# Performance work log

Hardware: AMD Instinct MI355X
Metric: run time of the kernel (lower is better)

## Reference

```python
import jax, jax.numpy as jnp
import numpy as np

B, T = 16, 8192
L, RC, DC, SC, EC, E, NC = 16, 32, 32, 256, 256, 100, 256


def conv1d(x, w, b, dilation=1):
    # x: [B, Cin, T], w: [Cout, Cin, K], b: [Cout]
    y = jax.lax.conv_general_dilated(
        x, w, window_strides=(1,), padding='VALID',
        rhs_dilation=(dilation,), dimension_numbers=('NCH', 'OIH', 'NCH'))
    return y + b[None, :, None]


def setup_inputs() -> dict:
    key = jax.random.key(0)
    ks = jax.random.split(key, 32)
    n = lambda k, shp: (jax.random.normal(k, shp) * 0.1).astype(jnp.float32)
    return dict(
        tokens=jax.random.randint(ks[0], (B, T), 0, NC),
        emb=n(ks[1], (NC, E)),
        init_w=n(ks[2], (RC, E, 1)), init_b=n(ks[3], (RC,)),
        dil_w=n(ks[4], (L, DC, RC, 2)), dil_b=n(ks[5], (L, DC)),
        filt_w=n(ks[6], (L, DC, DC, 2)), filt_b=n(ks[7], (L, DC)),
        gate_w=n(ks[8], (L, DC, DC, 2)), gate_b=n(ks[9], (L, DC)),
        res_w=n(ks[10], (L, RC, DC, 1)), res_b=n(ks[11], (L, RC)),
        skip_w=n(ks[12], (L, SC, DC, 1)), skip_b=n(ks[13], (L, SC)),
        end1_w=n(ks[14], (EC, SC, 1)), end1_b=n(ks[15], (EC,)),
        end2_w=n(ks[16], (EC, EC, 1)), end2_b=n(ks[17], (EC,)),
        fc1_w=n(ks[18], (128, 256)), fc1_b=n(ks[19], (128,)),
        fc2_w=n(ks[20], (128, 128)), fc2_b=n(ks[21], (128,)),
        fc3_w=n(ks[22], (64, 128)), fc3_b=n(ks[23], (64,)),
        fc4_w=n(ks[24], (NC, 64)), fc4_b=n(ks[25], (NC,)),
    )


def reference(tokens, emb, init_w, init_b, dil_w, dil_b, filt_w, filt_b,
              gate_w, gate_b, res_w, res_b, skip_w, skip_b,
              end1_w, end1_b, end2_w, end2_b,
              fc1_w, fc1_b, fc2_w, fc2_b, fc3_w, fc3_b, fc4_w, fc4_b):
    x = emb[tokens]                     # [B, T, E]
    x = jnp.transpose(x, (0, 2, 1))     # [B, E, T]
    x = conv1d(x, init_w, init_b)       # [B, RC, T]
    skip = None
    for i in range(L):
        d = 2 ** (i % 4)                # dilation resets each block of 4 layers
        xp = jnp.pad(x, ((0, 0), (0, 0), (d + 1, 0)))        # left pad d+1
        residual = conv1d(xp, dil_w[i], dil_b[i], dilation=d)  # [B, DC, T+1]
        f = jnp.tanh(conv1d(residual, filt_w[i], filt_b[i]))   # [B, DC, T]
        g = jax.nn.sigmoid(conv1d(residual, gate_w[i], gate_b[i]))
        x = f * g
        skip = conv1d(x, skip_w[i], skip_b[i])   # overwritten each layer (source bug, kept faithful)
        x = conv1d(x, res_w[i], res_b[i]) + residual[:, :, :-1]
    h = jax.nn.relu(conv1d(jax.nn.relu(skip), end1_w, end1_b))
    h = conv1d(h, end2_w, end2_b)       # [B, EC, T]
    h = h[:, :, -1]                     # [B, 256] last timestep only
    h = jax.nn.relu(h @ fc1_w.T + fc1_b)
    h = jax.nn.relu(h @ fc2_w.T + fc2_b)
    h = jax.nn.relu(h @ fc3_w.T + fc3_b)
    out = h @ fc4_w.T + fc4_b           # [B, NC]
    return out
```

## Files before the change

kernel.cpp:

```cpp
#include <hip/hip_runtime.h>


#define BB 16
#define TT 8192
#define LL 16
#define W0 77
#define NT 256

typedef __attribute__((ext_vector_type(8)))  short short8;
typedef __attribute__((ext_vector_type(16))) float float16;

#define MFMA_B16(a, b, c) __builtin_amdgcn_mfma_f32_32x32x16_bf16(a, b, c, 0, 0, 0)

__device__ __forceinline__ short f2bs(float f) {
  union { float ff; unsigned u; } v; v.ff = f;
  unsigned u = v.u;
  return (short)((u + 0x7FFFu + ((u >> 16) & 1u)) >> 16);
}
__device__ __forceinline__ float b2f(short h) {
  union { unsigned u; float f; } v;
  v.u = ((unsigned)(unsigned short)h) << 16; return v.f;
}
__device__ __forceinline__ float fast_sigmoid(float x) {
  return 1.f / (1.f + __expf(-x));
}
__device__ __forceinline__ float fast_tanh(float x) {
  return 2.f / (1.f + __expf(-2.f * x)) - 1.f;
}

__device__ __forceinline__ void afrag2(const short* src, int row, int kh, short8* out) {
  out[0] = *(const short8*)&src[row * 32 + 8 * kh];
  out[1] = *(const short8*)&src[row * 32 + 16 + 8 * kh];
}

__device__ __forceinline__ void stage_weights(
    int li, short* dst,
    const float* dil_w, const float* filt_w, const float* gate_w, const float* res_w,
    int t0, int nthr)
{
  for (int cid = t0; cid < 896; cid += nthr) {
    int mat = cid >> 7;
    int rem = cid & 127;
    int h = rem >> 6, ln = rem & 63;
    int n = ln & 31, k2 = ln >> 5;
    int base = (li * 32 + n) * 32 + 16 * h + 8 * k2;
    short8 v;
    if (mat == 6) {
      const float* p = res_w + base;
      #pragma unroll
      for (int j = 0; j < 8; j++) v[j] = f2bs(p[j]);
    } else {
      const float* w = (mat < 2) ? dil_w : (mat < 4) ? filt_w : gate_w;
      const float* p = w + base * 2 + (mat & 1);
      #pragma unroll
      for (int j = 0; j < 8; j++) v[j] = f2bs(p[2 * j]);
    }
    *(short8*)&dst[((mat * 2 + h) * 64 + ln) * 8] = v;
  }
}

__global__ __launch_bounds__(NT, 1) void wavenet_kernel(
    const int* __restrict__ tokens,
    const float* __restrict__ emb,
    const float* __restrict__ init_w, const float* __restrict__ init_b,
    const float* __restrict__ dil_w,  const float* __restrict__ dil_b,
    const float* __restrict__ filt_w, const float* __restrict__ filt_b,
    const float* __restrict__ gate_w, const float* __restrict__ gate_b,
    const float* __restrict__ res_w,  const float* __restrict__ res_b,
    const float* __restrict__ skip_w, const float* __restrict__ skip_b,
    const float* __restrict__ end1_w, const float* __restrict__ end1_b,
    const float* __restrict__ end2_w, const float* __restrict__ end2_b,
    const float* __restrict__ fc1_w,  const float* __restrict__ fc1_b,
    const float* __restrict__ fc2_w,  const float* __restrict__ fc2_b,
    const float* __restrict__ fc3_w,  const float* __restrict__ fc3_b,
    const float* __restrict__ fc4_w,  const float* __restrict__ fc4_b,
    float* __restrict__ out)
{
  __shared__ __align__(16) short bfw[2][7168];
  __shared__ float bias2[2][128];
  __shared__ __align__(16) short xbuf[W0 * 32];
  __shared__ __align__(16) short pool[8624];
  __shared__ int tok[W0];
  __shared__ float vecA[256], vecB[256];

  short* rb = pool;
  short* xm = pool + 2432;

  const int tid  = threadIdx.x;
  const int lane = tid & 63;
  const int wv   = tid >> 6;
  const int m    = lane & 31;
  const int kh   = lane >> 5;
  const int b    = blockIdx.x;

  if (tid < W0) tok[tid] = tokens[b * TT + (TT - 1 - tid)];
  __syncthreads();

  for (int cid = tid; cid < 77 * 14; cid += NT) {
    int u = cid / 14, s = cid % 14;
    const float* er = emb + tok[u] * 100 + s * 8;
    short8 v;
    if (s < 12) {
      #pragma unroll
      for (int j = 0; j < 8; j++) v[j] = f2bs(er[j]);
    } else if (s == 12) {
      #pragma unroll
      for (int j = 0; j < 4; j++) v[j] = f2bs(er[j]);
      #pragma unroll
      for (int j = 4; j < 8; j++) v[j] = 0;
    } else {
      #pragma unroll
      for (int j = 0; j < 8; j++) v[j] = 0;
    }
    *(short8*)&pool[u * 112 + s * 8] = v;
  }
  stage_weights(0, bfw[0], dil_w, filt_w, gate_w, res_w, tid, NT);
  if (tid < 128) {
    const float* bsrc = (tid < 32) ? dil_b : (tid < 64) ? filt_b : (tid < 96) ? gate_b : res_b;
    bias2[0][tid] = bsrc[tid & 31];
  }
  __syncthreads();

  if (wv == 0) {
    short8 bi[7];
    #pragma unroll
    for (int s = 0; s < 7; s++) {
      const float* p = init_w + m * 100 + s * 16 + kh * 8;
      short8 v;
      if (s < 6) {
        #pragma unroll
        for (int j = 0; j < 8; j++) v[j] = f2bs(p[j]);
      } else if (kh == 0) {
        #pragma unroll
        for (int j = 0; j < 4; j++) v[j] = f2bs(p[j]);
        #pragma unroll
        for (int j = 4; j < 8; j++) v[j] = 0;
      } else {
        #pragma unroll
        for (int j = 0; j < 8; j++) v[j] = 0;
      }
      bi[s] = v;
    }
    const float binit = init_b[m];
    int u = 0;
    #pragma unroll
    for (int t = 0; t < 3; t++) {
      int R = t * 32;
      u = R + m; if (u > 76) u = 76;
      float16 acc;
      #pragma unroll
      for (int r = 0; r < 16; r++) acc[r] = binit;
      #pragma unroll
      for (int s = 0; s < 7; s++) {
        short8 a = *(const short8*)&pool[u * 112 + s * 16 + kh * 8];
        acc = MFMA_B16(a, bi[s], acc);
      }
      #pragma unroll
      for (int r = 0; r < 16; r++) {
        int row = (r & 3) + 8 * (r >> 2) + 4 * kh;
        int uu = R + row;
        if (uu < W0) xbuf[uu * 32 + m] = f2bs(acc[r]);
      }
    }
  }

  int Win = W0;
  for (int i = 0; i < LL; i++) {
    __syncthreads();
    const int d = 1 << (i & 3);
    const int Wout = Win - d - 1;
    if (wv == 0) {
      const short* bw = bfw[i & 1];
      const float* bs = bias2[i & 1];
      short8 BW[7][2];
      #pragma unroll
      for (int mat = 0; mat < 7; mat++)
        #pragma unroll
        for (int h = 0; h < 2; h++)
          BW[mat][h] = *(const short8*)&bw[((mat * 2 + h) * 64 + lane) * 8];
      const int T1 = (Wout + 32) >> 5;
      const int T2 = (Wout + 31) >> 5;

      for (int t = 0; t < T1; t++) {
        int R = t * 32;
        int vra = R + m + d; if (vra > Win - 1) vra = Win - 1;
        int vrz = R + m;     if (vrz > Win - 1) vrz = Win - 1;
        short8 aA[2], aZ[2];
        afrag2(xbuf, vra, kh, aA);
        afrag2(xbuf, vrz, kh, aZ);
        float16 acc;
        const float bc = bs[m];
        #pragma unroll
        for (int r = 0; r < 16; r++) acc[r] = bc;
        acc = MFMA_B16(aA[0], BW[0][0], acc);
        acc = MFMA_B16(aA[1], BW[0][1], acc);
        acc = MFMA_B16(aZ[0], BW[1][0], acc);
        acc = MFMA_B16(aZ[1], BW[1][1], acc);
        #pragma unroll
        for (int r = 0; r < 16; r++) {
          int row = (r & 3) + 8 * (r >> 2) + 4 * kh;
          int vr = R + row;
          if (vr <= Wout) rb[vr * 32 + m] = f2bs(acc[r]);
        }
      }
      asm volatile("s_waitcnt lgkmcnt(0)" ::: "memory");

      for (int t = 0; t < T2; t++) {
        int R = t * 32;
        int r1 = R + m + 1; if (r1 > Wout) r1 = Wout;
        int r0 = R + m;     if (r0 > Wout) r0 = Wout;
        short8 a1[2], a0[2];
        afrag2(rb, r1, kh, a1);
        afrag2(rb, r0, kh, a0);
        float16 accF, accG;
        const float bf = bs[32 + m], bg = bs[64 + m];
        #pragma unroll
        for (int r = 0; r < 16; r++) { accF[r] = bf; accG[r] = bg; }
        accF = MFMA_B16(a1[0], BW[2][0], accF);
        accF = MFMA_B16(a1[1], BW[2][1], accF);
        accF = MFMA_B16(a0[0], BW[3][0], accF);
        accF = MFMA_B16(a0[1], BW[3][1], accF);
        accG = MFMA_B16(a1[0], BW[4][0], accG);
        accG = MFMA_B16(a1[1], BW[4][1], accG);
        accG = MFMA_B16(a0[0], BW[5][0], accG);
        accG = MFMA_B16(a0[1], BW[5][1], accG);
        #pragma unroll
        for (int r = 0; r < 16; r++) {
          int row = (r & 3) + 8 * (r >> 2) + 4 * kh;
          int uf = R + row;
          if (uf < Wout)
            xm[uf * 32 + m] = f2bs(fast_tanh(accF[r]) * fast_sigmoid(accG[r]));
        }
      }
      asm volatile("s_waitcnt lgkmcnt(0)" ::: "memory");

      for (int t = 0; t < T2; t++) {
        int R = t * 32;
        int rx = R + m; if (rx > Wout - 1) rx = Wout - 1;
        short8 aX[2];
        afrag2(xm, rx, kh, aX);
        float16 accX;
        const float br = bs[96 + m];
        #pragma unroll
        for (int r = 0; r < 16; r++) {
          int row = (r & 3) + 8 * (r >> 2) + 4 * kh;
          int rr = R + row + 1; if (rr > Wout) rr = Wout;
          accX[r] = br + b2f(rb[rr * 32 + m]);
        }
        accX = MFMA_B16(aX[0], BW[6][0], accX);
        accX = MFMA_B16(aX[1], BW[6][1], accX);
        #pragma unroll
        for (int r = 0; r < 16; r++) {
          int row = (r & 3) + 8 * (r >> 2) + 4 * kh;
          int uf = R + row;
          if (uf < Wout) xbuf[uf * 32 + m] = f2bs(accX[r]);
        }
      }
      asm volatile("s_waitcnt lgkmcnt(0)" ::: "memory");
    } else if (i + 1 < LL) {
      stage_weights(i + 1, bfw[(i + 1) & 1], dil_w, filt_w, gate_w, res_w,
                    tid - 64, 192);
      int idx = tid - 64;
      if (idx < 128) {
        const float* bsrc = (idx < 32) ? dil_b : (idx < 64) ? filt_b : (idx < 96) ? gate_b : res_b;
        bias2[(i + 1) & 1][idx] = bsrc[(i + 1) * 32 + (idx & 31)];
      }
    }
    Win = Wout;
  }
  __syncthreads();

  {
    float acc = skip_b[15 * 256 + tid];
    const float* wr = skip_w + (15 * 256 + tid) * 32;
    #pragma unroll
    for (int k = 0; k < 32; k += 4) {
      float4 w = *(const float4*)&wr[k];
      acc += (w.x * b2f(xm[k]) + w.y * b2f(xm[k+1])) + (w.z * b2f(xm[k+2]) + w.w * b2f(xm[k+3]));
    }
    vecA[tid] = fmaxf(acc, 0.f);
  }
  __syncthreads();
  {
    const float* wr = end1_w + tid * 256;
    float a4[4] = {0.f, 0.f, 0.f, 0.f};
    #pragma unroll 4
    for (int k = 0; k < 256; k += 16) {
      #pragma unroll
      for (int q = 0; q < 4; q++) {
        float4 w = *(const float4*)&wr[k + 4 * q];
        a4[q] += (w.x * vecA[k+4*q] + w.y * vecA[k+4*q+1]) + (w.z * vecA[k+4*q+2] + w.w * vecA[k+4*q+3]);
      }
    }
    vecB[tid] = fmaxf(end1_b[tid] + (a4[0] + a4[1]) + (a4[2] + a4[3]), 0.f);
  }
  __syncthreads();
  float h2;
  {
    const float* wr = end2_w + tid * 256;
    float a4[4] = {0.f, 0.f, 0.f, 0.f};
    #pragma unroll 4
    for (int k = 0; k < 256; k += 16) {
      #pragma unroll
      for (int q = 0; q < 4; q++) {
        float4 w = *(const float4*)&wr[k + 4 * q];
        a4[q] += (w.x * vecB[k+4*q] + w.y * vecB[k+4*q+1]) + (w.z * vecB[k+4*q+2] + w.w * vecB[k+4*q+3]);
      }
    }
    h2 = end2_b[tid] + (a4[0] + a4[1]) + (a4[2] + a4[3]);
  }
  __syncthreads();
  vecA[tid] = h2;
  __syncthreads();
  if (tid < 128) {
    const float* wr = fc1_w + tid * 256;
    float a4[4] = {0.f, 0.f, 0.f, 0.f};
    #pragma unroll 4
    for (int k = 0; k < 256; k += 16) {
      #pragma unroll
      for (int q = 0; q < 4; q++) {
        float4 w = *(const float4*)&wr[k + 4 * q];
        a4[q] += (w.x * vecA[k+4*q] + w.y * vecA[k+4*q+1]) + (w.z * vecA[k+4*q+2] + w.w * vecA[k+4*q+3]);
      }
    }
    vecB[tid] = fmaxf(fc1_b[tid] + (a4[0] + a4[1]) + (a4[2] + a4[3]), 0.f);
  }
  __syncthreads();
  if (tid < 128) {
    const float* wr = fc2_w + tid * 128;
    float a4[4] = {0.f, 0.f, 0.f, 0.f};
    #pragma unroll 2
    for (int k = 0; k < 128; k += 16) {
      #pragma unroll
      for (int q = 0; q < 4; q++) {
        float4 w = *(const float4*)&wr[k + 4 * q];
        a4[q] += (w.x * vecB[k+4*q] + w.y * vecB[k+4*q+1]) + (w.z * vecB[k+4*q+2] + w.w * vecB[k+4*q+3]);
      }
    }
    vecA[tid] = fmaxf(fc2_b[tid] + (a4[0] + a4[1]) + (a4[2] + a4[3]), 0.f);
  }
  __syncthreads();
  if (tid < 64) {
    const float* wr = fc3_w + tid * 128;
    float a4[4] = {0.f, 0.f, 0.f, 0.f};
    #pragma unroll 2
    for (int k = 0; k < 128; k += 16) {
      #pragma unroll
      for (int q = 0; q < 4; q++) {
        float4 w = *(const float4*)&wr[k + 4 * q];
        a4[q] += (w.x * vecA[k+4*q] + w.y * vecA[k+4*q+1]) + (w.z * vecA[k+4*q+2] + w.w * vecA[k+4*q+3]);
      }
    }
    vecB[tid] = fmaxf(fc3_b[tid] + (a4[0] + a4[1]) + (a4[2] + a4[3]), 0.f);
  }
  __syncthreads();
  {
    const float* wr = fc4_w + tid * 64;
    float a4[4] = {0.f, 0.f, 0.f, 0.f};
    #pragma unroll
    for (int k = 0; k < 64; k += 16) {
      #pragma unroll
      for (int q = 0; q < 4; q++) {
        float4 w = *(const float4*)&wr[k + 4 * q];
        a4[q] += (w.x * vecB[k+4*q] + w.y * vecB[k+4*q+1]) + (w.z * vecB[k+4*q+2] + w.w * vecB[k+4*q+3]);
      }
    }
    out[b * 256 + tid] = fc4_b[tid] + (a4[0] + a4[1]) + (a4[2] + a4[3]);
  }
}

extern "C" void kernel_launch(void* const* d_in, const int* in_sizes, int n_in,
                              void* d_out, int out_size, void* d_ws, size_t ws_size,
                              hipStream_t stream) {
  wavenet_kernel<<<BB, NT, 0, stream>>>(
      (const int*)d_in[0],    (const float*)d_in[1],  (const float*)d_in[2],  (const float*)d_in[3],
      (const float*)d_in[4],  (const float*)d_in[5],  (const float*)d_in[6],  (const float*)d_in[7],
      (const float*)d_in[8],  (const float*)d_in[9],  (const float*)d_in[10], (const float*)d_in[11],
      (const float*)d_in[12], (const float*)d_in[13], (const float*)d_in[14], (const float*)d_in[15],
      (const float*)d_in[16], (const float*)d_in[17], (const float*)d_in[18], (const float*)d_in[19],
      (const float*)d_in[20], (const float*)d_in[21], (const float*)d_in[22], (const float*)d_in[23],
      (const float*)d_in[24], (const float*)d_in[25], (float*)d_out);
}
```

Measured before the change: 228.9 us.

## Split layer time tiles across waves and prefetch next-layer weights into registers

Each layer's 32-row time tiles are now processed in parallel, one wave per tile, instead of wave 0 looping over them while the other waves only staged weights. Next-layer weights and biases are loaded from global memory into registers by all threads before the compute. They are converted to bf16 and written to shared memory afterwards, so the load latency overlaps with the MFMA work. This targets the serialized single-wave critical path in this latency-bound kernel, at the cost of an extra block barrier per layer and higher register pressure.

Result: faster. 212.2 us (-7.3%).

```diff
diff --git a/kernel.cpp b/kernel.cpp
--- a/kernel.cpp
+++ b/kernel.cpp
@@ -33,29 +33,23 @@
   out[1] = *(const short8*)&src[row * 32 + 16 + 8 * kh];
 }
 
-__device__ __forceinline__ void stage_weights(
-    int li, short* dst,
-    const float* dil_w, const float* filt_w, const float* gate_w, const float* res_w,
-    int t0, int nthr)
+__device__ __forceinline__ void load_chunk(
+    int li, int cid, float* pf,
+    const float* dil_w, const float* filt_w, const float* gate_w, const float* res_w)
 {
-  for (int cid = t0; cid < 896; cid += nthr) {
-    int mat = cid >> 7;
-    int rem = cid & 127;
-    int h = rem >> 6, ln = rem & 63;
-    int n = ln & 31, k2 = ln >> 5;
-    int base = (li * 32 + n) * 32 + 16 * h + 8 * k2;
-    short8 v;
-    if (mat == 6) {
-      const float* p = res_w + base;
-      #pragma unroll
-      for (int j = 0; j < 8; j++) v[j] = f2bs(p[j]);
-    } else {
-      const float* w = (mat < 2) ? dil_w : (mat < 4) ? filt_w : gate_w;
-      const float* p = w + base * 2 + (mat & 1);
-      #pragma unroll
-      for (int j = 0; j < 8; j++) v[j] = f2bs(p[2 * j]);
-    }
-    *(short8*)&dst[((mat * 2 + h) * 64 + ln) * 8] = v;
+  int mat = cid >> 7;
+  int h = (cid >> 6) & 1, ln = cid & 63;
+  int n = ln & 31, k2 = ln >> 5;
+  int base = (li * 32 + n) * 32 + 16 * h + 8 * k2;
+  if (mat == 6) {
+    const float* p = res_w + base;
+    #pragma unroll
+    for (int j = 0; j < 8; j++) pf[j] = p[j];
+  } else {
+    const float* w = (mat < 2) ? dil_w : (mat < 4) ? filt_w : gate_w;
+    const float* p = w + base * 2 + (mat & 1);
+    #pragma unroll
+    for (int j = 0; j < 8; j++) pf[j] = p[2 * j];
   }
 }
 
@@ -114,7 +108,14 @@
     }
     *(short8*)&pool[u * 112 + s * 8] = v;
   }
-  stage_weights(0, bfw[0], dil_w, filt_w, gate_w, res_w, tid, NT);
+  for (int cid = tid; cid < 896; cid += NT) {
+    float pf[8];
+    load_chunk(0, cid, pf, dil_w, filt_w, gate_w, res_w);
+    short8 v;
+    #pragma unroll
+    for (int j = 0; j < 8; j++) v[j] = f2bs(pf[j]);
+    *(short8*)&bfw[0][cid * 8] = v;
+  }
   if (tid < 128) {
     const float* bsrc = (tid < 32) ? dil_b : (tid < 64) ? filt_b : (tid < 96) ? gate_b : res_b;
     bias2[0][tid] = bsrc[tid & 31];
@@ -142,11 +143,10 @@
       bi[s] = v;
     }
     const float binit = init_b[m];
-    int u = 0;
     #pragma unroll
     for (int t = 0; t < 3; t++) {
       int R = t * 32;
-      u = R + m; if (u > 76) u = 76;
+      int u = R + m; if (u > 76) u = 76;
       float16 acc;
       #pragma unroll
       for (int r = 0; r < 16; r++) acc[r] = binit;
@@ -163,112 +163,132 @@
       }
     }
   }
+  __syncthreads();
 
   int Win = W0;
   for (int i = 0; i < LL; i++) {
-    __syncthreads();
     const int d = 1 << (i & 3);
     const int Wout = Win - d - 1;
-    if (wv == 0) {
-      const short* bw = bfw[i & 1];
-      const float* bs = bias2[i & 1];
-      short8 BW[7][2];
-      #pragma unroll
-      for (int mat = 0; mat < 7; mat++)
+    const int T = (Wout + 32) >> 5;
+    const short* bw = bfw[i & 1];
+    const float* bs = bias2[i & 1];
+
+    float pf[4][8];
+    float pbias = 0.f;
+    const int nch = (tid < 128) ? 4 : 3;
+    if (i + 1 < LL) {
+      #pragma unroll
+      for (int q = 0; q < 4; q++) {
+        if (q < nch)
+          load_chunk(i + 1, tid + q * NT, pf[q], dil_w, filt_w, gate_w, res_w);
+      }
+      if (tid < 128) {
+        const float* bsrc = (tid < 32) ? dil_b : (tid < 64) ? filt_b : (tid < 96) ? gate_b : res_b;
+        pbias = bsrc[(i + 1) * 32 + (tid & 31)];
+      }
+    }
+
+    if (wv < T) {
+      const int R = wv * 32;
+      short8 B0[2], B1[2];
+      #pragma unroll
+      for (int h = 0; h < 2; h++) {
+        B0[h] = *(const short8*)&bfw[i & 1][((0 * 2 + h) * 64 + lane) * 8];
+        B1[h] = *(const short8*)&bfw[i & 1][((1 * 2 + h) * 64 + lane) * 8];
+      }
+      int vra = R + m + d; if (vra > Win - 1) vra = Win - 1;
+      int vrz = R + m;     if (vrz > Win - 1) vrz = Win - 1;
+      short8 aA[2], aZ[2];
+      afrag2(xbuf, vra, kh, aA);
+      afrag2(xbuf, vrz, kh, aZ);
+      float16 acc;
+      const float bc = bs[m];
+      #pragma unroll
+      for (int r = 0; r < 16; r++) acc[r] = bc;
+      acc = MFMA_B16(aA[0], B0[0], acc);
+      acc = MFMA_B16(aA[1], B0[1], acc);
+      acc = MFMA_B16(aZ[0], B1[0], acc);
+      acc = MFMA_B16(aZ[1], B1[1], acc);
+      #pragma unroll
+      for (int r = 0; r < 16; r++) {
+        int row = (r & 3) + 8 * (r >> 2) + 4 * kh;
+        int vr = R + row;
+        if (vr <= Wout) rb[vr * 32 + m] = f2bs(acc[r]);
+      }
+    }
+    __syncthreads();
+
+    if (wv < T) {
+      const int R = wv * 32;
+      short8 BW[5][2];
+      #pragma unroll
+      for (int mt = 0; mt < 5; mt++)
         #pragma unroll
         for (int h = 0; h < 2; h++)
-          BW[mat][h] = *(const short8*)&bw[((mat * 2 + h) * 64 + lane) * 8];
-      const int T1 = (Wout + 32) >> 5;
-      const int T2 = (Wout + 31) >> 5;
-
-      for (int t = 0; t < T1; t++) {
-        int R = t * 32;
-        int vra = R + m + d; if (vra > Win - 1) vra = Win - 1;
-        int vrz = R + m;     if (vrz > Win - 1) vrz = Win - 1;
-        short8 aA[2], aZ[2];
-        afrag2(xbuf, vra, kh, aA);
-        afrag2(xbuf, vrz, kh, aZ);
-        float16 acc;
-        const float bc = bs[m];
-        #pragma unroll
-        for (int r = 0; r < 16; r++) acc[r] = bc;
-        acc = MFMA_B16(aA[0], BW[0][0], acc);
-        acc = MFMA_B16(aA[1], BW[0][1], acc);
-        acc = MFMA_B16(aZ[0], BW[1][0], acc);
-        acc = MFMA_B16(aZ[1], BW[1][1], acc);
-        #pragma unroll
-        for (int r = 0; r < 16; r++) {
-          int row = (r & 3) + 8 * (r >> 2) + 4 * kh;
-          int vr = R + row;
-          if (vr <= Wout) rb[vr * 32 + m] = f2bs(acc[r]);
+          BW[mt][h] = *(const short8*)&bw[(((mt + 2) * 2 + h) * 64 + lane) * 8];
+      int r1 = R + m + 1; if (r1 > Wout) r1 = Wout;
+      int r0 = R + m;     if (r0 > Wout) r0 = Wout;
+      short8 a1[2], a0[2];
+      afrag2(rb, r1, kh, a1);
+      afrag2(rb, r0, kh, a0);
+      float16 accF, accG;
+      const float bf = bs[32 + m], bg = bs[64 + m];
+      #pragma unroll
+      for (int r = 0; r < 16; r++) { accF[r] = bf; accG[r] = bg; }
+      accF = MFMA_B16(a1[0], BW[0][0], accF);
+      accF = MFMA_B16(a1[1], BW[0][1], accF);
+      accF = MFMA_B16(a0[0], BW[1][0], accF);
+      accF = MFMA_B16(a0[1], BW[1][1], accF);
+      accG = MFMA_B16(a1[0], BW[2][0], accG);
+      accG = MFMA_B16(a1[1], BW[2][1], accG);
+      accG = MFMA_B16(a0[0], BW[3][0], accG);
+      accG = MFMA_B16(a0[1], BW[3][1], accG);
+      #pragma unroll
+      for (int r = 0; r < 16; r++) {
+        int row = (r & 3) + 8 * (r >> 2) + 4 * kh;
+        int uf = R + row;
+        if (uf < Wout)
+          xm[uf * 32 + m] = f2bs(fast_tanh(accF[r]) * fast_sigmoid(accG[r]));
+      }
+      asm volatile("s_waitcnt lgkmcnt(0)" ::: "memory");
+
+      int rx = R + m; if (rx > Wout - 1) rx = Wout - 1;
+      short8 aX[2];
+      afrag2(xm, rx, kh, aX);
+      float16 accX;
+      const float br = bs[96 + m];
+      #pragma unroll
+      for (int r = 0; r < 16; r++) {
+        int row = (r & 3) + 8 * (r >> 2) + 4 * kh;
+        int rr = R + row + 1; if (rr > Wout) rr = Wout;
+        accX[r] = br + b2f(rb[rr * 32 + m]);
+      }
+      accX = MFMA_B16(aX[0], BW[4][0], accX);
+      accX = MFMA_B16(aX[1], BW[4][1], accX);
+      #pragma unroll
+      for (int r = 0; r < 16; r++) {
+        int row = (r & 3) + 8 * (r >> 2) + 4 * kh;
+        int uf = R + row;
+        if (uf < Wout) xbuf[uf * 32 + m] = f2bs(accX[r]);
+      }
+    }
+
+    if (i + 1 < LL) {
+      short* dst = bfw[(i + 1) & 1];
+      #pragma unroll
+      for (int q = 0; q < 4; q++) {
+        if (q < nch) {
+          short8 v;
+          #pragma unroll
+          for (int j = 0; j < 8; j++) v[j] = f2bs(pf[q][j]);
+          *(short8*)&dst[(tid + q * NT) * 8] = v;
         }
       }
-      asm volatile("s_waitcnt lgkmcnt(0)" ::: "memory");
-
-      for (int t = 0; t < T2; t++) {
-        int R = t * 32;
-        int r1 = R + m + 1; if (r1 > Wout) r1 = Wout;
-        int r0 = R + m;     if (r0 > Wout) r0 = Wout;
-        short8 a1[2], a0[2];
-        afrag2(rb, r1, kh, a1);
-        afrag2(rb, r0, kh, a0);
-        float16 accF, accG;
-        const float bf = bs[32 + m], bg = bs[64 + m];
-        #pragma unroll
-        for (int r = 0; r < 16; r++) { accF[r] = bf; accG[r] = bg; }
-        accF = MFMA_B16(a1[0], BW[2][0], accF);
-        accF = MFMA_B16(a1[1], BW[2][1], accF);
-        accF = MFMA_B16(a0[0], BW[3][0], accF);
-        accF = MFMA_B16(a0[1], BW[3][1], accF);
-        accG = MFMA_B16(a1[0], BW[4][0], accG);
-        accG = MFMA_B16(a1[1], BW[4][1], accG);
-        accG = MFMA_B16(a0[0], BW[5][0], accG);
-        accG = MFMA_B16(a0[1], BW[5][1], accG);
-        #pragma unroll
-        for (int r = 0; r < 16; r++) {
-          int row = (r & 3) + 8 * (r >> 2) + 4 * kh;
-          int uf = R + row;
-          if (uf < Wout)
-            xm[uf * 32 + m] = f2bs(fast_tanh(accF[r]) * fast_sigmoid(accG[r]));
-        }
-      }
-      asm volatile("s_waitcnt lgkmcnt(0)" ::: "memory");
-
-      for (int t = 0; t < T2; t++) {
-        int R = t * 32;
-        int rx = R + m; if (rx > Wout - 1) rx = Wout - 1;
-        short8 aX[2];
-        afrag2(xm, rx, kh, aX);
-        float16 accX;
-        const float br = bs[96 + m];
-        #pragma unroll
-        for (int r = 0; r < 16; r++) {
-          int row = (r & 3) + 8 * (r >> 2) + 4 * kh;
-          int rr = R + row + 1; if (rr > Wout) rr = Wout;
-          accX[r] = br + b2f(rb[rr * 32 + m]);
-        }
-        accX = MFMA_B16(aX[0], BW[6][0], accX);
-        accX = MFMA_B16(aX[1], BW[6][1], accX);
-        #pragma unroll
-        for (int r = 0; r < 16; r++) {
-          int row = (r & 3) + 8 * (r >> 2) + 4 * kh;
-          int uf = R + row;
-          if (uf < Wout) xbuf[uf * 32 + m] = f2bs(accX[r]);
-        }
-      }
-      asm volatile("s_waitcnt lgkmcnt(0)" ::: "memory");
-    } else if (i + 1 < LL) {
-      stage_weights(i + 1, bfw[(i + 1) & 1], dil_w, filt_w, gate_w, res_w,
-                    tid - 64, 192);
-      int idx = tid - 64;
-      if (idx < 128) {
-        const float* bsrc = (idx < 32) ? dil_b : (idx < 64) ? filt_b : (idx < 96) ? gate_b : res_b;
-        bias2[(i + 1) & 1][idx] = bsrc[(i + 1) * 32 + (idx & 31)];
-      }
-    }
+      if (tid < 128) bias2[(i + 1) & 1][tid] = pbias;
+    }
+    __syncthreads();
     Win = Wout;
   }
-  __syncthreads();
 
   {
     float acc = skip_b[15 * 256 + tid];
```
